# Optimization experiments

Measured on AMD Instinct MI355X. Metric: run time of the kernel, lower is better.

The kernel has to match this reference:

```python
import jax, jax.numpy as jnp
import numpy as np

HID = 128
EPS = 0.05
SHARP = 50.0


def _linear_init(key, fan_in, fan_out):
    # torch nn.Linear default: U(-1/sqrt(fan_in), 1/sqrt(fan_in)) for W and b
    kw, kb = jax.random.split(key)
    bound = 1.0 / np.sqrt(fan_in)
    W = jax.random.uniform(kw, (fan_in, fan_out), jnp.float32, -bound, bound)
    b = jax.random.uniform(kb, (fan_out,), jnp.float32, -bound, bound)
    return W, b


def setup_inputs() -> dict:
    key = jax.random.key(0)
    keys = jax.random.split(key, 7)
    N = 1048576
    xy = jax.random.uniform(keys[0], (N, 2), jnp.float32)  # collocation points in unit square
    U = jnp.ones((1,), jnp.float32)
    W1, b1 = _linear_init(keys[1], 2, HID)
    W2, b2 = _linear_init(keys[2], HID, HID)
    W3, b3 = _linear_init(keys[3], HID, HID)
    W4, b4 = _linear_init(keys[4], HID, HID)
    W5, b5 = _linear_init(keys[5], HID, 2)
    return {"xy": xy, "U": U, "W1": W1, "b1": b1, "W2": W2, "b2": b2,
            "W3": W3, "b3": b3, "W4": W4, "b4": b4, "W5": W5, "b5": b5}


def reference(xy, U, W1, b1, W2, b2, W3, b3, W4, b4, W5, b5):
    h = jnp.tanh(xy @ W1 + b1)
    h = jnp.tanh(h @ W2 + b2)
    h = jnp.tanh(h @ W3 + b3)
    h = jnp.tanh(h @ W4 + b4)
    out = h @ W5 + b5                      # [N, 2]
    u_hat, v_hat = out[:, 0], out[:, 1]
    x, y = xy[:, 0], xy[:, 1]
    psi = jax.nn.sigmoid(SHARP * (x - EPS)) * jax.nn.sigmoid(SHARP * (1.0 - EPS - x))
    B = x * (1.0 - x) * y * (1.0 - y)      # boundary bump
    u = U * y * psi + B * u_hat
    v = B * v_hat
    return (u, v)
```

## Files before the change

kernel.cpp:

```cpp
#include <hip/hip_runtime.h>
#include <hip/hip_bf16.h>

#define NPTS  1048576
#define GRID  512
#define NTILE 8192
#define C2    2.8853900817779268f

typedef __attribute__((ext_vector_type(8))) short  s16x8;
typedef __attribute__((ext_vector_type(4))) float  f32x4;

#define KEEP(x) asm volatile("" : "+v"(x))

__device__ __forceinline__ unsigned short bf16r(float v) {
  unsigned u = __builtin_bit_cast(unsigned, v);
  return (unsigned short)((u + 0x7fffu + ((u >> 16) & 1u)) >> 16);
}
__device__ __forceinline__ unsigned pack_bf16x2(float lo, float hi) {
  __hip_bfloat162 h = __float22bfloat162_rn(float2{lo, hi});
  unsigned r;
  __builtin_memcpy(&r, &h, sizeof(r));
  return r;
}
__device__ __forceinline__ float tanh_e(float acc, float bc) {
  float e = __builtin_amdgcn_exp2f(fmaf(acc, C2, bc));
  return 1.0f - 2.0f * __builtin_amdgcn_rcpf(1.0f + e);
}
__device__ __forceinline__ float sigm_fast(float x) {
  return __builtin_amdgcn_rcpf(1.0f + __builtin_amdgcn_exp2f(x * -1.4426950408889634f));
}

__global__ void prep_kernel(const float* __restrict__ W2, const float* __restrict__ W3,
                            const float* __restrict__ W4, const float* __restrict__ W5,
                            unsigned short* __restrict__ ws)
{
  int tid = blockIdx.x * 256 + threadIdx.x;
  if (tid < 49152) {
    int l    = tid >> 14;
    int idx  = tid & 16383;
    int e    = idx & 7;
    int lane = (idx >> 3) & 63;
    int kt   = (idx >> 9) & 3;
    int nbg  = (idx >> 11) & 7;
    int k = kt * 32 + (lane >> 4) * 8 + e;
    int n = nbg * 16 + (lane & 15);
    const float* W = (l == 0) ? W2 : (l == 1) ? W3 : W4;
    ws[tid] = bf16r(W[k * 128 + n]);
  } else if (tid < 49664) {
    int idx  = tid - 49152;
    int e    = idx & 7;
    int lane = (idx >> 3) & 63;
    int kt   = idx >> 9;
    int k  = kt * 32 + (lane >> 4) * 8 + e;
    int nl = lane & 15;
    ws[tid] = (nl < 2) ? bf16r(W5[k * 2 + nl]) : (unsigned short)0;
  }
}

__global__ __launch_bounds__(256, 2)
void mlp_kernel(const float* __restrict__ xy, const float* __restrict__ Uin,
                const float* __restrict__ W1, const float* __restrict__ b1,
                const float* __restrict__ b2, const float* __restrict__ b3,
                const float* __restrict__ b4, const float* __restrict__ b5,
                const unsigned short* __restrict__ ws, float* __restrict__ out)
{
  __shared__ __align__(16) unsigned char hbuf0[32768];
  __shared__ __align__(16) unsigned char hbuf1[32768];

  const int tid  = threadIdx.x;
  const int lane = tid & 63;
  const int wid  = tid >> 6;
  const int lg   = lane >> 4;
  const int ln   = lane & 15;
  const int o    = tid >> 4;
  const int c0   = tid & 15;

  const float Uval = Uin[0];
  const float b50  = b5[0];
  const float b51  = b5[1];

  float bcr[3][2][4];
#pragma unroll
  for (int nb = 0; nb < 2; ++nb)
#pragma unroll
    for (int r = 0; r < 4; ++r) {
      int n = wid * 32 + nb * 16 + lg * 4 + r;
      bcr[0][nb][r] = b2[n] * C2;
      bcr[1][nb][r] = b3[n] * C2;
      bcr[2][nb][r] = b4[n] * C2;
    }

  float w1x[8], w1y[8], b1r[8];
#pragma unroll
  for (int t = 0; t < 8; ++t) {
    w1x[t] = W1[o * 8 + t];
    w1y[t] = W1[128 + o * 8 + t];
    b1r[t] = b1[o * 8 + t];
  }

  s16x8 Wa[3][2][4];
#pragma unroll
  for (int l = 0; l < 3; ++l)
#pragma unroll
    for (int nb = 0; nb < 2; ++nb)
#pragma unroll
      for (int kt = 0; kt < 4; ++kt) {
        Wa[l][nb][kt] = *(const s16x8*)(ws + (((l * 8 + wid * 2 + nb) * 4 + kt) << 9) + lane * 8);
        KEEP(Wa[l][nb][kt]);
      }
  s16x8 b5f[4];
#pragma unroll
  for (int kt = 0; kt < 4; ++kt) {
    b5f[kt] = *(const s16x8*)(ws + 49152 + kt * 512 + lane * 8);
    KEEP(b5f[kt]);
  }

  const unsigned rBase  = (unsigned)(lane * 16);
  const unsigned wBase0 = (unsigned)(wid * 1024 + ((lg >> 1)) * 256 + ln * 16 + (lg & 1) * 8);
  const unsigned wBase1 = wBase0 + 512;
  const unsigned l1Base = (unsigned)((o >> 2) * 1024 + (o & 3) * 256 + c0 * 16);

  for (int tile = blockIdx.x; tile < NTILE; tile += GRID) {
    const int pbase = tile << 7;

#pragma unroll
    for (int i = 0; i < 8; ++i) {
      int p = i * 16 + c0;
      float2 v = ((const float2*)xy)[pbase + p];
      unsigned q[4];
#pragma unroll
      for (int t2 = 0; t2 < 4; ++t2) {
        float s0 = fmaf(v.x, w1x[2 * t2],     fmaf(v.y, w1y[2 * t2],     b1r[2 * t2]));
        float s1 = fmaf(v.x, w1x[2 * t2 + 1], fmaf(v.y, w1y[2 * t2 + 1], b1r[2 * t2 + 1]));
        float e0 = __builtin_amdgcn_exp2f(s0 * C2);
        float e1 = __builtin_amdgcn_exp2f(s1 * C2);
        float h0 = 1.0f - 2.0f * __builtin_amdgcn_rcpf(1.0f + e0);
        float h1 = 1.0f - 2.0f * __builtin_amdgcn_rcpf(1.0f + e1);
        q[t2] = pack_bf16x2(h0, h1);
      }
      *(uint4*)(hbuf0 + l1Base + i * 4096) = uint4{q[0], q[1], q[2], q[3]};
    }
    __syncthreads();

#pragma unroll
    for (int l = 0; l < 3; ++l) {
      const unsigned char* bufR = (l & 1) ? hbuf1 : hbuf0;
      unsigned char*       bufW = (l & 1) ? hbuf0 : hbuf1;
#pragma unroll
      for (int mt = 0; mt < 8; ++mt) {
        s16x8 B[4];
#pragma unroll
        for (int kt = 0; kt < 4; ++kt)
          B[kt] = *(const s16x8*)(bufR + rBase + mt * 4096 + kt * 1024);
        f32x4 acc0 = f32x4{0.f, 0.f, 0.f, 0.f};
        f32x4 acc1 = f32x4{0.f, 0.f, 0.f, 0.f};
#pragma unroll
        for (int kt = 0; kt < 4; ++kt) {
          acc0 = __builtin_amdgcn_mfma_f32_16x16x32_bf16(Wa[l][0][kt], B[kt], acc0, 0, 0, 0);
          acc1 = __builtin_amdgcn_mfma_f32_16x16x32_bf16(Wa[l][1][kt], B[kt], acc1, 0, 0, 0);
        }
        {
          float t0 = tanh_e(acc0[0], bcr[l][0][0]);
          float t1 = tanh_e(acc0[1], bcr[l][0][1]);
          float t2 = tanh_e(acc0[2], bcr[l][0][2]);
          float t3 = tanh_e(acc0[3], bcr[l][0][3]);
          *(uint2*)(bufW + wBase0 + mt * 4096) = uint2{pack_bf16x2(t0, t1), pack_bf16x2(t2, t3)};
        }
        {
          float t0 = tanh_e(acc1[0], bcr[l][1][0]);
          float t1 = tanh_e(acc1[1], bcr[l][1][1]);
          float t2 = tanh_e(acc1[2], bcr[l][1][2]);
          float t3 = tanh_e(acc1[3], bcr[l][1][3]);
          *(uint2*)(bufW + wBase1 + mt * 4096) = uint2{pack_bf16x2(t0, t1), pack_bf16x2(t2, t3)};
        }
      }
      __syncthreads();
    }

    f32x4 acc5[2];
#pragma unroll
    for (int m5 = 0; m5 < 2; ++m5) acc5[m5] = f32x4{0.f, 0.f, 0.f, 0.f};
#pragma unroll
    for (int m5 = 0; m5 < 2; ++m5)
#pragma unroll
      for (int kt = 0; kt < 4; ++kt) {
        s16x8 b = *(const s16x8*)(hbuf1 + rBase + (wid * 2 + m5) * 4096 + kt * 1024);
        acc5[m5] = __builtin_amdgcn_mfma_f32_16x16x32_bf16(b5f[kt], b, acc5[m5], 0, 0, 0);
      }
    if (lg == 0) {
#pragma unroll
      for (int m5 = 0; m5 < 2; ++m5) {
        int p = pbase + wid * 32 + m5 * 16 + ln;
        float uh = acc5[m5][0] + b50;
        float vh = acc5[m5][1] + b51;
        float2 v = ((const float2*)xy)[p];
        float Bm = v.x * (1.0f - v.x) * v.y * (1.0f - v.y);
        float psi = sigm_fast(50.0f * (v.x - 0.05f)) * sigm_fast(50.0f * (0.95f - v.x));
        out[p]        = fmaf(Uval * v.y, psi, Bm * uh);
        out[NPTS + p] = Bm * vh;
      }
    }
  }
}

extern "C" void kernel_launch(void* const* d_in, const int* in_sizes, int n_in,
                              void* d_out, int out_size, void* d_ws, size_t ws_size,
                              hipStream_t stream) {
  const float* xy = (const float*)d_in[0];
  const float* U  = (const float*)d_in[1];
  const float* W1 = (const float*)d_in[2];
  const float* b1 = (const float*)d_in[3];
  const float* W2 = (const float*)d_in[4];
  const float* b2 = (const float*)d_in[5];
  const float* W3 = (const float*)d_in[6];
  const float* b3 = (const float*)d_in[7];
  const float* W4 = (const float*)d_in[8];
  const float* b4 = (const float*)d_in[9];
  const float* W5 = (const float*)d_in[10];
  const float* b5 = (const float*)d_in[11];
  unsigned short* ws = (unsigned short*)d_ws;
  float* out = (float*)d_out;

  prep_kernel<<<194, 256, 0, stream>>>(W2, W3, W4, W5, ws);
  mlp_kernel<<<GRID, 256, 0, stream>>>(xy, U, W1, b1, b2, b3, b4, b5, ws, out);
}
```

Measured before the change: 208.1 us.

## Halve tile size, stream weights from memory, and raise occupancy to five blocks

Shrinks each tile from 128 to 64 points, halving the LDS ping-pong buffers, and stops holding all three layers' MFMA weight fragments in registers. Weights are now reloaded from global memory (likely L1/L2 hits) inside the inner MFMA loop. The grid rises to 1280 blocks and launch bounds allow 5 blocks per CU, aiming to hide latency through occupancy. The cost is many repeated global weight loads per tile and less MFMA work between barriers.

```diff
diff --git a/kernel.cpp b/kernel.cpp
--- a/kernel.cpp
+++ b/kernel.cpp
@@ -2,14 +2,12 @@
 #include <hip/hip_bf16.h>
 
 #define NPTS  1048576
-#define GRID  512
-#define NTILE 8192
+#define GRID  1280
+#define NTILE 16384
 #define C2    2.8853900817779268f
 
 typedef __attribute__((ext_vector_type(8))) short  s16x8;
 typedef __attribute__((ext_vector_type(4))) float  f32x4;
-
-#define KEEP(x) asm volatile("" : "+v"(x))
 
 __device__ __forceinline__ unsigned short bf16r(float v) {
   unsigned u = __builtin_bit_cast(unsigned, v);
@@ -56,15 +54,15 @@
   }
 }
 
-__global__ __launch_bounds__(256, 2)
+__global__ __launch_bounds__(256, 5)
 void mlp_kernel(const float* __restrict__ xy, const float* __restrict__ Uin,
                 const float* __restrict__ W1, const float* __restrict__ b1,
                 const float* __restrict__ b2, const float* __restrict__ b3,
                 const float* __restrict__ b4, const float* __restrict__ b5,
                 const unsigned short* __restrict__ ws, float* __restrict__ out)
 {
-  __shared__ __align__(16) unsigned char hbuf0[32768];
-  __shared__ __align__(16) unsigned char hbuf1[32768];
+  __shared__ __align__(16) unsigned char hbuf0[16384];
+  __shared__ __align__(16) unsigned char hbuf1[16384];
 
   const int tid  = threadIdx.x;
   const int lane = tid & 63;
@@ -97,33 +95,21 @@
     b1r[t] = b1[o * 8 + t];
   }
 
-  s16x8 Wa[3][2][4];
-#pragma unroll
-  for (int l = 0; l < 3; ++l)
-#pragma unroll
-    for (int nb = 0; nb < 2; ++nb)
-#pragma unroll
-      for (int kt = 0; kt < 4; ++kt) {
-        Wa[l][nb][kt] = *(const s16x8*)(ws + (((l * 8 + wid * 2 + nb) * 4 + kt) << 9) + lane * 8);
-        KEEP(Wa[l][nb][kt]);
-      }
   s16x8 b5f[4];
 #pragma unroll
-  for (int kt = 0; kt < 4; ++kt) {
+  for (int kt = 0; kt < 4; ++kt)
     b5f[kt] = *(const s16x8*)(ws + 49152 + kt * 512 + lane * 8);
-    KEEP(b5f[kt]);
-  }
 
   const unsigned rBase  = (unsigned)(lane * 16);
-  const unsigned wBase0 = (unsigned)(wid * 1024 + ((lg >> 1)) * 256 + ln * 16 + (lg & 1) * 8);
+  const unsigned wBase0 = (unsigned)(wid * 1024 + (lg >> 1) * 256 + ln * 16 + (lg & 1) * 8);
   const unsigned wBase1 = wBase0 + 512;
   const unsigned l1Base = (unsigned)((o >> 2) * 1024 + (o & 3) * 256 + c0 * 16);
 
   for (int tile = blockIdx.x; tile < NTILE; tile += GRID) {
-    const int pbase = tile << 7;
-
-#pragma unroll
-    for (int i = 0; i < 8; ++i) {
+    const int pbase = tile << 6;
+
+#pragma unroll
+    for (int i = 0; i < 4; ++i) {
       int p = i * 16 + c0;
       float2 v = ((const float2*)xy)[pbase + p];
       unsigned q[4];
@@ -146,7 +132,7 @@
       const unsigned char* bufR = (l & 1) ? hbuf1 : hbuf0;
       unsigned char*       bufW = (l & 1) ? hbuf0 : hbuf1;
 #pragma unroll
-      for (int mt = 0; mt < 8; ++mt) {
+      for (int mt = 0; mt < 4; ++mt) {
         s16x8 B[4];
 #pragma unroll
         for (int kt = 0; kt < 4; ++kt)
@@ -155,8 +141,10 @@
         f32x4 acc1 = f32x4{0.f, 0.f, 0.f, 0.f};
 #pragma unroll
         for (int kt = 0; kt < 4; ++kt) {
-          acc0 = __builtin_amdgcn_mfma_f32_16x16x32_bf16(Wa[l][0][kt], B[kt], acc0, 0, 0, 0);
-          acc1 = __builtin_amdgcn_mfma_f32_16x16x32_bf16(Wa[l][1][kt], B[kt], acc1, 0, 0, 0);
+          s16x8 Wa0 = *(const s16x8*)(ws + (((l * 8 + wid * 2 + 0) * 4 + kt) << 9) + lane * 8);
+          s16x8 Wa1 = *(const s16x8*)(ws + (((l * 8 + wid * 2 + 1) * 4 + kt) << 9) + lane * 8);
+          acc0 = __builtin_amdgcn_mfma_f32_16x16x32_bf16(Wa0, B[kt], acc0, 0, 0, 0);
+          acc1 = __builtin_amdgcn_mfma_f32_16x16x32_bf16(Wa1, B[kt], acc1, 0, 0, 0);
         }
         {
           float t0 = tanh_e(acc0[0], bcr[l][0][0]);
@@ -176,28 +164,21 @@
       __syncthreads();
     }
 
-    f32x4 acc5[2];
-#pragma unroll
-    for (int m5 = 0; m5 < 2; ++m5) acc5[m5] = f32x4{0.f, 0.f, 0.f, 0.f};
-#pragma unroll
-    for (int m5 = 0; m5 < 2; ++m5)
-#pragma unroll
-      for (int kt = 0; kt < 4; ++kt) {
-        s16x8 b = *(const s16x8*)(hbuf1 + rBase + (wid * 2 + m5) * 4096 + kt * 1024);
-        acc5[m5] = __builtin_amdgcn_mfma_f32_16x16x32_bf16(b5f[kt], b, acc5[m5], 0, 0, 0);
-      }
+    f32x4 acc5 = f32x4{0.f, 0.f, 0.f, 0.f};
+#pragma unroll
+    for (int kt = 0; kt < 4; ++kt) {
+      s16x8 b = *(const s16x8*)(hbuf1 + rBase + wid * 4096 + kt * 1024);
+      acc5 = __builtin_amdgcn_mfma_f32_16x16x32_bf16(b5f[kt], b, acc5, 0, 0, 0);
+    }
     if (lg == 0) {
-#pragma unroll
-      for (int m5 = 0; m5 < 2; ++m5) {
-        int p = pbase + wid * 32 + m5 * 16 + ln;
-        float uh = acc5[m5][0] + b50;
-        float vh = acc5[m5][1] + b51;
-        float2 v = ((const float2*)xy)[p];
-        float Bm = v.x * (1.0f - v.x) * v.y * (1.0f - v.y);
-        float psi = sigm_fast(50.0f * (v.x - 0.05f)) * sigm_fast(50.0f * (0.95f - v.x));
-        out[p]        = fmaf(Uval * v.y, psi, Bm * uh);
-        out[NPTS + p] = Bm * vh;
-      }
+      int p = pbase + wid * 16 + ln;
+      float uh = acc5[0] + b50;
+      float vh = acc5[1] + b51;
+      float2 v = ((const float2*)xy)[p];
+      float Bm = v.x * (1.0f - v.x) * v.y * (1.0f - v.y);
+      float psi = sigm_fast(50.0f * (v.x - 0.05f)) * sigm_fast(50.0f * (0.95f - v.x));
+      out[p]        = fmaf(Uval * v.y, psi, Bm * uh);
+      out[NPTS + p] = Bm * vh;
     }
   }
 }
```

Measured after the change: 376.3 us. +80.8%, slower.
